# Kernel optimization log

Measured on AMD Instinct MI355X. Metric: run time of the kernel, lower is better.

## Reference

```python
import jax, jax.numpy as jnp
import numpy as np

# Math note: feat = cat([ctx_i, asp_j, ctx_i*asp_j]) dotted with w_u [6H,1]
# decomposes as ctx_i.w1 + asp_j.w2 + (ctx_i*asp_j).w3 where w_u = cat([w1,w2,w3]).
# This lets us compute the full [B, L1, L2] alignment matrix with three small
# contractions instead of L1*L2 concat+matmul launches, with identical math.

def setup_inputs() -> dict:
    key = jax.random.key(0)
    k1, k2, k3 = jax.random.split(key, 3)
    B, L1, L2, D = 64, 512, 32, 600  # D = 2*hidden_dim
    ctx = jax.random.normal(k1, (B, L1, D), dtype=jnp.float32)
    asp = jax.random.normal(k2, (B, L2, D), dtype=jnp.float32)
    w_u = jax.random.normal(k3, (3 * D, 1), dtype=jnp.float32)
    return {"batch_size": B, "ctx": ctx, "asp": asp, "w_u": w_u}

def reference(batch_size, ctx, asp, w_u):
    D = ctx.shape[-1]
    w = w_u[:, 0]
    w1, w2, w3 = w[:D], w[D:2 * D], w[2 * D:]
    ctx_term = ctx @ w1                                  # [B, L1]
    asp_term = asp @ w2                                  # [B, L2]
    cross = jnp.einsum('bid,bjd->bij', ctx * w3, asp)    # [B, L1, L2]
    return ctx_term[:, :, None] + asp_term[:, None, :] + cross
```

## Files before the change

kernel.cpp:

```cpp
#include <hip/hip_runtime.h>
#include <hip/hip_bf16.h>

typedef float  f32x4  __attribute__((ext_vector_type(4)));
typedef short  bf16x8 __attribute__((ext_vector_type(8)));
typedef short  s16x4  __attribute__((ext_vector_type(4)));

#define NB   64
#define NL1  512
#define NL2  32
#define ND   600
#define NDP  640
#define NW1  608
#define ROWS 64

static __device__ __forceinline__ short f2bf(float f) {
    __hip_bfloat16 h = __float2bfloat16(f);
    return __builtin_bit_cast(short, h);
}

__global__ __launch_bounds__(256, 2)
void align_kernel(const float* __restrict__ ctx,
                  const float* __restrict__ asp,
                  const float* __restrict__ wu,
                  float* __restrict__ out)
{
    __shared__ short aspw3[NL2 * NDP];
    __shared__ short w1bf[NW1];
    __shared__ float aspterm[NL2];

    const int tid     = threadIdx.x;
    const int lane    = tid & 63;
    const int wid     = tid >> 6;
    const int b       = blockIdx.x;
    const int rowbase = blockIdx.y * ROWS;

    const int r16 = lane & 15;
    const int g   = lane >> 4;
    const int jx  = lane & 7;
    const float* actx = ctx + ((size_t)b * NL1 + rowbase + wid * 16 + r16) * ND + 8 * g;

    float4 v0 = *(const float4*)(actx);
    float4 v1 = *(const float4*)(actx + 4);
    float4 n0 = *(const float4*)(actx + 32);
    float4 n1 = *(const float4*)(actx + 36);

    for (int i = tid; i < NW1; i += 256)
        w1bf[i] = (i < ND) ? f2bf(wu[i]) : (short)0;

    {
        const int j   = tid >> 3;
        const int e   = tid & 7;
        const int jxs = j & 7;

        aspw3[j * NDP + ((75 ^ jxs) << 3) + e] = 0;

        const int sub = tid & 7;
        const float* arow = asp + ((size_t)b * NL2 + j) * ND;
        float at = 0.f;
        #pragma unroll
        for (int m = 0; m < 19; ++m) {
            const int k = m * 32 + sub * 4;
            if (k < ND) {
                const float4 v  = *(const float4*)(arow + k);
                const float4 w2 = *(const float4*)(wu + ND + k);
                const float4 w3 = *(const float4*)(wu + 2 * ND + k);
                at += v.x * w2.x + v.y * w2.y + v.z * w2.z + v.w * w2.w;
                s16x4 h;
                h.x = f2bf(v.x * w3.x);
                h.y = f2bf(v.y * w3.y);
                h.z = f2bf(v.z * w3.z);
                h.w = f2bf(v.w * w3.w);
                const int c = (k >> 3) ^ jxs;
                *(s16x4*)&aspw3[j * NDP + (c << 3) + (k & 7)] = h;
            }
        }
        at += __shfl_xor(at, 1);
        at += __shfl_xor(at, 2);
        at += __shfl_xor(at, 4);
        if (sub == 0) aspterm[j] = at;
    }
    __syncthreads();

    f32x4 acc0 = {0.f, 0.f, 0.f, 0.f};
    f32x4 acc1 = {0.f, 0.f, 0.f, 0.f};
    f32x4 acc2 = {0.f, 0.f, 0.f, 0.f};

    #pragma unroll 1
    for (int s = 0; s < 19; ++s) {
        float4 p0 = make_float4(0.f, 0.f, 0.f, 0.f);
        float4 p1 = make_float4(0.f, 0.f, 0.f, 0.f);
        if (s < 16) {
            p0 = *(const float4*)(actx + (s + 2) * 32);
            p1 = *(const float4*)(actx + (s + 2) * 32 + 4);
        } else if (s == 16) {
            if (g < 3) {
                p0 = *(const float4*)(actx + 18 * 32);
                p1 = *(const float4*)(actx + 18 * 32 + 4);
            }
        }

        const int k0 = s * 32;
        bf16x8 af;
        af[0] = f2bf(v0.x); af[1] = f2bf(v0.y); af[2] = f2bf(v0.z); af[3] = f2bf(v0.w);
        af[4] = f2bf(v1.x); af[5] = f2bf(v1.y); af[6] = f2bf(v1.z); af[7] = f2bf(v1.w);
        const int c = ((s * 4 + g) ^ jx) << 3;
        const bf16x8 b0 = *(const bf16x8*)&aspw3[r16 * NDP + c];
        const bf16x8 b1 = *(const bf16x8*)&aspw3[(16 + r16) * NDP + c];
        const bf16x8 wf = *(const bf16x8*)&w1bf[k0 + 8 * g];
        acc0 = __builtin_amdgcn_mfma_f32_16x16x32_bf16(af, b0, acc0, 0, 0, 0);
        acc1 = __builtin_amdgcn_mfma_f32_16x16x32_bf16(af, b1, acc1, 0, 0, 0);
        acc2 = __builtin_amdgcn_mfma_f32_16x16x32_bf16(af, wf, acc2, 0, 0, 0);

        v0 = n0; v1 = n1;
        n0 = p0; n1 = p1;
    }

    const float atj0 = aspterm[r16];
    const float atj1 = aspterm[16 + r16];
    float* orow = out + ((size_t)b * NL1 + rowbase + wid * 16 + g * 4) * NL2;
    #pragma unroll
    for (int r = 0; r < 4; ++r) {
        const float cterm = acc2[r];
        orow[r * NL2 + r16]      = acc0[r] + cterm + atj0;
        orow[r * NL2 + 16 + r16] = acc1[r] + cterm + atj1;
    }
}

extern "C" void kernel_launch(void* const* d_in, const int* in_sizes, int n_in,
                              void* d_out, int out_size, void* d_ws, size_t ws_size,
                              hipStream_t stream) {
    (void)in_sizes; (void)n_in; (void)d_ws; (void)ws_size; (void)out_size;
    const float* ctx = (const float*)d_in[1];
    const float* asp = (const float*)d_in[2];
    const float* wu  = (const float*)d_in[3];
    float* out = (float*)d_out;
    dim3 grid(NB, NL1 / ROWS);
    align_kernel<<<grid, 256, 0, stream>>>(ctx, asp, wu, out);
}
```

Measured before the change: 21.84 us.

## Split K across two waves and stream asp from global instead of LDS staging

Replaces the per-block LDS staging of bf16 asp*w3 with direct global loads of asp fragments. The w3 scaling moves onto the ctx operand, and the asp term is computed via an extra MFMA against w2. Blocks shrink to 16 rows and 128 threads, with the two waves splitting the K dimension and reducing through a small LDS buffer. This removes the serial staging prologue and raises occupancy. In exchange, asp is re-read by many more blocks and each wave does more bf16 conversions per step.

```diff
diff --git a/kernel.cpp b/kernel.cpp
--- a/kernel.cpp
+++ b/kernel.cpp
@@ -3,126 +3,127 @@
 
 typedef float  f32x4  __attribute__((ext_vector_type(4)));
 typedef short  bf16x8 __attribute__((ext_vector_type(8)));
-typedef short  s16x4  __attribute__((ext_vector_type(4)));
 
 #define NB   64
 #define NL1  512
 #define NL2  32
 #define ND   600
-#define NDP  640
-#define NW1  608
-#define ROWS 64
+#define NW   608
 
 static __device__ __forceinline__ short f2bf(float f) {
     __hip_bfloat16 h = __float2bfloat16(f);
     return __builtin_bit_cast(short, h);
 }
 
-__global__ __launch_bounds__(256, 2)
+__global__ __launch_bounds__(128, 4)
 void align_kernel(const float* __restrict__ ctx,
                   const float* __restrict__ asp,
                   const float* __restrict__ wu,
                   float* __restrict__ out)
 {
-    __shared__ short aspw3[NL2 * NDP];
-    __shared__ short w1bf[NW1];
-    __shared__ float aspterm[NL2];
+    __shared__ short w1bf[NW];
+    __shared__ short w2bf[NW];
+    __shared__ float w3s[NW];
+    __shared__ float comb[64][15];
 
     const int tid     = threadIdx.x;
     const int lane    = tid & 63;
-    const int wid     = tid >> 6;
+    const int kh      = tid >> 6;
     const int b       = blockIdx.x;
-    const int rowbase = blockIdx.y * ROWS;
+    const int rowbase = blockIdx.y * 16;
 
     const int r16 = lane & 15;
     const int g   = lane >> 4;
-    const int jx  = lane & 7;
-    const float* actx = ctx + ((size_t)b * NL1 + rowbase + wid * 16 + r16) * ND + 8 * g;
 
-    float4 v0 = *(const float4*)(actx);
-    float4 v1 = *(const float4*)(actx + 4);
-    float4 n0 = *(const float4*)(actx + 32);
-    float4 n1 = *(const float4*)(actx + 36);
+    const float* actx = ctx + ((size_t)b * NL1 + rowbase + r16) * ND + 8 * g;
+    const float* aspb = asp + ((size_t)b * NL2 + r16) * ND + 8 * g;
 
-    for (int i = tid; i < NW1; i += 256)
-        w1bf[i] = (i < ND) ? f2bf(wu[i]) : (short)0;
+    const int sbeg = kh ? 10 : 0;
+    const int send = kh ? 19 : 10;
 
-    {
-        const int j   = tid >> 3;
-        const int e   = tid & 7;
-        const int jxs = j & 7;
+#define ISSUE(t, C0, C1, A0, A1, B0, B1)                                   \
+    if ((t) <= 17 || ((t) == 18 && g < 3)) {                               \
+        C0 = *(const float4*)(actx + (t) * 32);                            \
+        C1 = *(const float4*)(actx + (t) * 32 + 4);                        \
+        A0 = *(const float4*)(aspb + (t) * 32);                            \
+        A1 = *(const float4*)(aspb + (t) * 32 + 4);                        \
+        B0 = *(const float4*)(aspb + 16 * ND + (t) * 32);                  \
+        B1 = *(const float4*)(aspb + 16 * ND + (t) * 32 + 4);              \
+    } else {                                                               \
+        C0 = C1 = A0 = A1 = B0 = B1 = make_float4(0.f, 0.f, 0.f, 0.f);    \
+    }
 
-        aspw3[j * NDP + ((75 ^ jxs) << 3) + e] = 0;
+    float4 c0, c1, a0, a1, b0, b1;
+    ISSUE(sbeg, c0, c1, a0, a1, b0, b1)
 
-        const int sub = tid & 7;
-        const float* arow = asp + ((size_t)b * NL2 + j) * ND;
-        float at = 0.f;
-        #pragma unroll
-        for (int m = 0; m < 19; ++m) {
-            const int k = m * 32 + sub * 4;
-            if (k < ND) {
-                const float4 v  = *(const float4*)(arow + k);
-                const float4 w2 = *(const float4*)(wu + ND + k);
-                const float4 w3 = *(const float4*)(wu + 2 * ND + k);
-                at += v.x * w2.x + v.y * w2.y + v.z * w2.z + v.w * w2.w;
-                s16x4 h;
-                h.x = f2bf(v.x * w3.x);
-                h.y = f2bf(v.y * w3.y);
-                h.z = f2bf(v.z * w3.z);
-                h.w = f2bf(v.w * w3.w);
-                const int c = (k >> 3) ^ jxs;
-                *(s16x4*)&aspw3[j * NDP + (c << 3) + (k & 7)] = h;
-            }
-        }
-        at += __shfl_xor(at, 1);
-        at += __shfl_xor(at, 2);
-        at += __shfl_xor(at, 4);
-        if (sub == 0) aspterm[j] = at;
+    for (int i = tid; i < NW; i += 128) {
+        const bool v = i < ND;
+        w1bf[i] = v ? f2bf(wu[i])        : (short)0;
+        w2bf[i] = v ? f2bf(wu[ND + i])   : (short)0;
+        w3s[i]  = v ? wu[2 * ND + i]     : 0.f;
     }
     __syncthreads();
 
-    f32x4 acc0 = {0.f, 0.f, 0.f, 0.f};
-    f32x4 acc1 = {0.f, 0.f, 0.f, 0.f};
-    f32x4 acc2 = {0.f, 0.f, 0.f, 0.f};
+    f32x4 acc0 = {0,0,0,0};
+    f32x4 acc1 = {0,0,0,0};
+    f32x4 acc2 = {0,0,0,0};
+    f32x4 acc3 = {0,0,0,0};
+    f32x4 acc4 = {0,0,0,0};
 
     #pragma unroll 1
-    for (int s = 0; s < 19; ++s) {
-        float4 p0 = make_float4(0.f, 0.f, 0.f, 0.f);
-        float4 p1 = make_float4(0.f, 0.f, 0.f, 0.f);
-        if (s < 16) {
-            p0 = *(const float4*)(actx + (s + 2) * 32);
-            p1 = *(const float4*)(actx + (s + 2) * 32 + 4);
-        } else if (s == 16) {
-            if (g < 3) {
-                p0 = *(const float4*)(actx + 18 * 32);
-                p1 = *(const float4*)(actx + 18 * 32 + 4);
-            }
+    for (int s = sbeg; s < send; ++s) {
+        float4 nc0, nc1, na0, na1, nb0, nb1;
+        ISSUE(s + 1, nc0, nc1, na0, na1, nb0, nb1)
+
+        const int k0g = s * 32 + 8 * g;
+        const bf16x8 wf  = *(const bf16x8*)&w1bf[k0g];
+        const bf16x8 w2f = *(const bf16x8*)&w2bf[k0g];
+        const float4 w3a = *(const float4*)&w3s[k0g];
+        const float4 w3b = *(const float4*)&w3s[k0g + 4];
+
+        bf16x8 af, afw, f0, f1;
+        af[0]  = f2bf(c0.x);        af[1]  = f2bf(c0.y);
+        af[2]  = f2bf(c0.z);        af[3]  = f2bf(c0.w);
+        af[4]  = f2bf(c1.x);        af[5]  = f2bf(c1.y);
+        af[6]  = f2bf(c1.z);        af[7]  = f2bf(c1.w);
+        afw[0] = f2bf(c0.x * w3a.x); afw[1] = f2bf(c0.y * w3a.y);
+        afw[2] = f2bf(c0.z * w3a.z); afw[3] = f2bf(c0.w * w3a.w);
+        afw[4] = f2bf(c1.x * w3b.x); afw[5] = f2bf(c1.y * w3b.y);
+        afw[6] = f2bf(c1.z * w3b.z); afw[7] = f2bf(c1.w * w3b.w);
+        f0[0] = f2bf(a0.x); f0[1] = f2bf(a0.y); f0[2] = f2bf(a0.z); f0[3] = f2bf(a0.w);
+        f0[4] = f2bf(a1.x); f0[5] = f2bf(a1.y); f0[6] = f2bf(a1.z); f0[7] = f2bf(a1.w);
+        f1[0] = f2bf(b0.x); f1[1] = f2bf(b0.y); f1[2] = f2bf(b0.z); f1[3] = f2bf(b0.w);
+        f1[4] = f2bf(b1.x); f1[5] = f2bf(b1.y); f1[6] = f2bf(b1.z); f1[7] = f2bf(b1.w);
+
+        acc0 = __builtin_amdgcn_mfma_f32_16x16x32_bf16(afw, f0, acc0, 0, 0, 0);
+        acc1 = __builtin_amdgcn_mfma_f32_16x16x32_bf16(afw, f1, acc1, 0, 0, 0);
+        acc2 = __builtin_amdgcn_mfma_f32_16x16x32_bf16(af,  wf, acc2, 0, 0, 0);
+        acc3 = __builtin_amdgcn_mfma_f32_16x16x32_bf16(w2f, f0, acc3, 0, 0, 0);
+        acc4 = __builtin_amdgcn_mfma_f32_16x16x32_bf16(w2f, f1, acc4, 0, 0, 0);
+
+        c0 = nc0; c1 = nc1; a0 = na0; a1 = na1; b0 = nb0; b1 = nb1;
+    }
+#undef ISSUE
+
+    if (kh == 1) {
+        float* c = comb[lane];
+        c[0]  = acc0[0]; c[1]  = acc0[1]; c[2]  = acc0[2]; c[3]  = acc0[3];
+        c[4]  = acc1[0]; c[5]  = acc1[1]; c[6]  = acc1[2]; c[7]  = acc1[3];
+        c[8]  = acc2[0]; c[9]  = acc2[1]; c[10] = acc2[2]; c[11] = acc2[3];
+        c[12] = acc3[0]; c[13] = acc4[0];
+    }
+    __syncthreads();
+    if (kh == 0) {
+        const float* c = comb[lane];
+        const float atj0 = acc3[0] + c[12];
+        const float atj1 = acc4[0] + c[13];
+        float* orow = out + ((size_t)b * NL1 + rowbase + g * 4) * NL2;
+        #pragma unroll
+        for (int r = 0; r < 4; ++r) {
+            const float ct = acc2[r] + c[8 + r];
+            orow[r * NL2 + r16]      = acc0[r] + c[r]     + ct + atj0;
+            orow[r * NL2 + 16 + r16] = acc1[r] + c[4 + r] + ct + atj1;
         }
-
-        const int k0 = s * 32;
-        bf16x8 af;
-        af[0] = f2bf(v0.x); af[1] = f2bf(v0.y); af[2] = f2bf(v0.z); af[3] = f2bf(v0.w);
-        af[4] = f2bf(v1.x); af[5] = f2bf(v1.y); af[6] = f2bf(v1.z); af[7] = f2bf(v1.w);
-        const int c = ((s * 4 + g) ^ jx) << 3;
-        const bf16x8 b0 = *(const bf16x8*)&aspw3[r16 * NDP + c];
-        const bf16x8 b1 = *(const bf16x8*)&aspw3[(16 + r16) * NDP + c];
-        const bf16x8 wf = *(const bf16x8*)&w1bf[k0 + 8 * g];
-        acc0 = __builtin_amdgcn_mfma_f32_16x16x32_bf16(af, b0, acc0, 0, 0, 0);
-        acc1 = __builtin_amdgcn_mfma_f32_16x16x32_bf16(af, b1, acc1, 0, 0, 0);
-        acc2 = __builtin_amdgcn_mfma_f32_16x16x32_bf16(af, wf, acc2, 0, 0, 0);
-
-        v0 = n0; v1 = n1;
-        n0 = p0; n1 = p1;
-    }
-
-    const float atj0 = aspterm[r16];
-    const float atj1 = aspterm[16 + r16];
-    float* orow = out + ((size_t)b * NL1 + rowbase + wid * 16 + g * 4) * NL2;
-    #pragma unroll
-    for (int r = 0; r < 4; ++r) {
-        const float cterm = acc2[r];
-        orow[r * NL2 + r16]      = acc0[r] + cterm + atj0;
-        orow[r * NL2 + 16 + r16] = acc1[r] + cterm + atj1;
     }
 }
 
@@ -134,6 +135,6 @@
     const float* asp = (const float*)d_in[2];
     const float* wu  = (const float*)d_in[3];
     float* out = (float*)d_out;
-    dim3 grid(NB, NL1 / ROWS);
-    align_kernel<<<grid, 256, 0, stream>>>(ctx, asp, wu, out);
+    dim3 grid(NB, NL1 / 16);
+    align_kernel<<<grid, 128, 0, stream>>>(ctx, asp, wu, out);
 }
```

Result: slower. 28.01 us (+28.2%).

## Split asp/w3 prep into separate kernel writing MFMA-ready bf16 panels

Applied to the files above, without the earlier changes.

Adds a prep kernel that builds per-batch bf16 asp*w3 panels, the bf16 w1 vector and partial asp·w2 sums in workspace, laid out in MFMA fragment order. The main kernel then loads B fragments straight from global memory instead of having every block redo the prep in LDS behind a __syncthreads. The main loop is unrolled by two with double-buffered register prefetch. This removes prep work repeated 8x per batch and the LDS barrier, but adds a second launch and a workspace round trip.

```diff
diff --git a/kernel.cpp b/kernel.cpp
--- a/kernel.cpp
+++ b/kernel.cpp
@@ -9,115 +9,158 @@
 #define NL1  512
 #define NL2  32
 #define ND   600
-#define NDP  640
-#define NW1  608
-#define ROWS 64
+#define PBATCH 19456
+#define PANEL_SH ((size_t)NB * PBATCH)
+#define W1P_OFF  PANEL_SH
+#define AT4_OFF  (PANEL_SH + 608)
 
 static __device__ __forceinline__ short f2bf(float f) {
     __hip_bfloat16 h = __float2bfloat16(f);
     return __builtin_bit_cast(short, h);
 }
 
+__global__ __launch_bounds__(256, 4)
+void prep_kernel(const float* __restrict__ asp,
+                 const float* __restrict__ wu,
+                 short* __restrict__ ws_sh)
+{
+    short* panel = ws_sh;
+    short* w1p   = ws_sh + W1P_OFF;
+    float* at4   = (float*)(ws_sh + AT4_OFF);
+
+    const int b    = blockIdx.x;
+    const int q    = blockIdx.y;
+    const int sbeg = q * 5;
+    const int send = (q == 3) ? 19 : sbeg + 5;
+    const int tid  = threadIdx.x;
+    const int j    = tid >> 3;
+    const int sub  = tid & 7;
+    const int gq   = sub >> 1;
+    const int e4   = (sub & 1) * 4;
+    const int half = j >> 4;
+    const int r    = j & 15;
+
+    const float* arow = asp + ((size_t)b * NL2 + j) * ND;
+    short* pb = panel + (size_t)b * PBATCH;
+
+    float at = 0.f;
+    #pragma unroll
+    for (int s = sbeg; s < send; ++s) {
+        const int k = s * 32 + sub * 4;
+        if (k < ND) {
+            const float4 v  = *(const float4*)(arow + k);
+            const float4 w2 = *(const float4*)(wu + ND + k);
+            const float4 w3 = *(const float4*)(wu + 2 * ND + k);
+            at += v.x * w2.x + v.y * w2.y + v.z * w2.z + v.w * w2.w;
+            s16x4 h;
+            h.x = f2bf(v.x * w3.x);
+            h.y = f2bf(v.y * w3.y);
+            h.z = f2bf(v.z * w3.z);
+            h.w = f2bf(v.w * w3.w);
+            *(s16x4*)&pb[(((s * 2 + half) * 4 + gq) * 16 + r) * 8 + e4] = h;
+        }
+    }
+    at += __shfl_xor(at, 1);
+    at += __shfl_xor(at, 2);
+    at += __shfl_xor(at, 4);
+    if (sub == 0) at4[((size_t)b * 4 + q) * NL2 + j] = at;
+
+    if (q == 3) {
+        if (tid < 32) {
+            const int hh = tid >> 4, rr = tid & 15;
+            #pragma unroll
+            for (int e = 0; e < 8; ++e)
+                pb[(((18 * 2 + hh) * 4 + 3) * 16 + rr) * 8 + e] = 0;
+        }
+        if (b == 0 && tid < 76) {
+            const int s = tid >> 2, gg = tid & 3;
+            #pragma unroll
+            for (int e = 0; e < 8; ++e) {
+                const int k = s * 32 + gg * 8 + e;
+                w1p[(s * 4 + gg) * 8 + e] = (k < ND) ? f2bf(wu[k]) : (short)0;
+            }
+        }
+    }
+}
+
 __global__ __launch_bounds__(256, 2)
 void align_kernel(const float* __restrict__ ctx,
-                  const float* __restrict__ asp,
-                  const float* __restrict__ wu,
+                  const short* __restrict__ ws_sh,
                   float* __restrict__ out)
 {
-    __shared__ short aspw3[NL2 * NDP];
-    __shared__ short w1bf[NW1];
-    __shared__ float aspterm[NL2];
+    const short* panel = ws_sh;
+    const short* w1p   = ws_sh + W1P_OFF;
+    const float* at4   = (const float*)(ws_sh + AT4_OFF);
 
     const int tid     = threadIdx.x;
     const int lane    = tid & 63;
     const int wid     = tid >> 6;
     const int b       = blockIdx.x;
-    const int rowbase = blockIdx.y * ROWS;
+    const int rowbase = blockIdx.y * 64 + wid * 16;
 
     const int r16 = lane & 15;
     const int g   = lane >> 4;
-    const int jx  = lane & 7;
-    const float* actx = ctx + ((size_t)b * NL1 + rowbase + wid * 16 + r16) * ND + 8 * g;
 
-    float4 v0 = *(const float4*)(actx);
-    float4 v1 = *(const float4*)(actx + 4);
-    float4 n0 = *(const float4*)(actx + 32);
-    float4 n1 = *(const float4*)(actx + 36);
+    const float* actx = ctx + ((size_t)b * NL1 + rowbase + r16) * ND + 8 * g;
+    const short* pb   = panel + (size_t)b * PBATCH;
 
-    for (int i = tid; i < NW1; i += 256)
-        w1bf[i] = (i < ND) ? f2bf(wu[i]) : (short)0;
+#define ISSUE_C(t, C0, C1)                                                     \
+    if ((t) <= 17 || ((t) == 18 && g < 3)) {                                   \
+        C0 = *(const float4*)(actx + (t) * 32);                                \
+        C1 = *(const float4*)(actx + (t) * 32 + 4);                            \
+    } else if ((t) == 18) {                                                    \
+        C0 = make_float4(0.f, 0.f, 0.f, 0.f);                                  \
+        C1 = make_float4(0.f, 0.f, 0.f, 0.f);                                  \
+    }
 
-    {
-        const int j   = tid >> 3;
-        const int e   = tid & 7;
-        const int jxs = j & 7;
+#define ISSUE_B(t, F0, F1, WF)                                                 \
+    if ((t) <= 18) {                                                           \
+        F0 = *(const bf16x8*)&pb[(t) * 1024 + lane * 8];                       \
+        F1 = *(const bf16x8*)&pb[(t) * 1024 + 512 + lane * 8];                 \
+        WF = *(const bf16x8*)&w1p[((t) * 4 + g) * 8];                          \
+    }
 
-        aspw3[j * NDP + ((75 ^ jxs) << 3) + e] = 0;
+    float4 cA0, cA1, cB0, cB1;
+    bf16x8 fA0, fA1, wA, fB0, fB1, wB;
+    ISSUE_C(0, cA0, cA1) ISSUE_B(0, fA0, fA1, wA)
+    ISSUE_C(1, cB0, cB1) ISSUE_B(1, fB0, fB1, wB)
 
-        const int sub = tid & 7;
-        const float* arow = asp + ((size_t)b * NL2 + j) * ND;
-        float at = 0.f;
-        #pragma unroll
-        for (int m = 0; m < 19; ++m) {
-            const int k = m * 32 + sub * 4;
-            if (k < ND) {
-                const float4 v  = *(const float4*)(arow + k);
-                const float4 w2 = *(const float4*)(wu + ND + k);
-                const float4 w3 = *(const float4*)(wu + 2 * ND + k);
-                at += v.x * w2.x + v.y * w2.y + v.z * w2.z + v.w * w2.w;
-                s16x4 h;
-                h.x = f2bf(v.x * w3.x);
-                h.y = f2bf(v.y * w3.y);
-                h.z = f2bf(v.z * w3.z);
-                h.w = f2bf(v.w * w3.w);
-                const int c = (k >> 3) ^ jxs;
-                *(s16x4*)&aspw3[j * NDP + (c << 3) + (k & 7)] = h;
-            }
-        }
-        at += __shfl_xor(at, 1);
-        at += __shfl_xor(at, 2);
-        at += __shfl_xor(at, 4);
-        if (sub == 0) aspterm[j] = at;
+    f32x4 acc0 = {0,0,0,0};
+    f32x4 acc1 = {0,0,0,0};
+    f32x4 acc2 = {0,0,0,0};
+
+#define STEP(s, C0, C1, F0, F1, WF)                                            \
+    {                                                                          \
+        bf16x8 af;                                                             \
+        af[0] = f2bf(C0.x); af[1] = f2bf(C0.y);                                \
+        af[2] = f2bf(C0.z); af[3] = f2bf(C0.w);                                \
+        af[4] = f2bf(C1.x); af[5] = f2bf(C1.y);                                \
+        af[6] = f2bf(C1.z); af[7] = f2bf(C1.w);                                \
+        acc0 = __builtin_amdgcn_mfma_f32_16x16x32_bf16(af, F0, acc0, 0, 0, 0); \
+        acc1 = __builtin_amdgcn_mfma_f32_16x16x32_bf16(af, F1, acc1, 0, 0, 0); \
+        acc2 = __builtin_amdgcn_mfma_f32_16x16x32_bf16(af, WF, acc2, 0, 0, 0); \
+        ISSUE_C((s) + 2, C0, C1)                                               \
+        ISSUE_B((s) + 2, F0, F1, WF)                                           \
     }
-    __syncthreads();
-
-    f32x4 acc0 = {0.f, 0.f, 0.f, 0.f};
-    f32x4 acc1 = {0.f, 0.f, 0.f, 0.f};
-    f32x4 acc2 = {0.f, 0.f, 0.f, 0.f};
 
     #pragma unroll 1
-    for (int s = 0; s < 19; ++s) {
-        float4 p0 = make_float4(0.f, 0.f, 0.f, 0.f);
-        float4 p1 = make_float4(0.f, 0.f, 0.f, 0.f);
-        if (s < 16) {
-            p0 = *(const float4*)(actx + (s + 2) * 32);
-            p1 = *(const float4*)(actx + (s + 2) * 32 + 4);
-        } else if (s == 16) {
-            if (g < 3) {
-                p0 = *(const float4*)(actx + 18 * 32);
-                p1 = *(const float4*)(actx + 18 * 32 + 4);
-            }
-        }
+    for (int s = 0; s < 18; s += 2) {
+        STEP(s,     cA0, cA1, fA0, fA1, wA)
+        STEP(s + 1, cB0, cB1, fB0, fB1, wB)
+    }
+    STEP(18, cA0, cA1, fA0, fA1, wA)
 
-        const int k0 = s * 32;
-        bf16x8 af;
-        af[0] = f2bf(v0.x); af[1] = f2bf(v0.y); af[2] = f2bf(v0.z); af[3] = f2bf(v0.w);
-        af[4] = f2bf(v1.x); af[5] = f2bf(v1.y); af[6] = f2bf(v1.z); af[7] = f2bf(v1.w);
-        const int c = ((s * 4 + g) ^ jx) << 3;
-        const bf16x8 b0 = *(const bf16x8*)&aspw3[r16 * NDP + c];
-        const bf16x8 b1 = *(const bf16x8*)&aspw3[(16 + r16) * NDP + c];
-        const bf16x8 wf = *(const bf16x8*)&w1bf[k0 + 8 * g];
-        acc0 = __builtin_amdgcn_mfma_f32_16x16x32_bf16(af, b0, acc0, 0, 0, 0);
-        acc1 = __builtin_amdgcn_mfma_f32_16x16x32_bf16(af, b1, acc1, 0, 0, 0);
-        acc2 = __builtin_amdgcn_mfma_f32_16x16x32_bf16(af, wf, acc2, 0, 0, 0);
+#undef STEP
+#undef ISSUE_B
+#undef ISSUE_C
 
-        v0 = n0; v1 = n1;
-        n0 = p0; n1 = p1;
+    float atj0 = 0.f, atj1 = 0.f;
+    #pragma unroll
+    for (int q = 0; q < 4; ++q) {
+        atj0 += at4[((size_t)b * 4 + q) * NL2 + r16];
+        atj1 += at4[((size_t)b * 4 + q) * NL2 + 16 + r16];
     }
-
-    const float atj0 = aspterm[r16];
-    const float atj1 = aspterm[16 + r16];
-    float* orow = out + ((size_t)b * NL1 + rowbase + wid * 16 + g * 4) * NL2;
+    float* orow = out + ((size_t)b * NL1 + rowbase + g * 4) * NL2;
     #pragma unroll
     for (int r = 0; r < 4; ++r) {
         const float cterm = acc2[r];
@@ -129,11 +172,15 @@
 extern "C" void kernel_launch(void* const* d_in, const int* in_sizes, int n_in,
                               void* d_out, int out_size, void* d_ws, size_t ws_size,
                               hipStream_t stream) {
-    (void)in_sizes; (void)n_in; (void)d_ws; (void)ws_size; (void)out_size;
+    (void)in_sizes; (void)n_in; (void)ws_size; (void)out_size;
     const float* ctx = (const float*)d_in[1];
     const float* asp = (const float*)d_in[2];
     const float* wu  = (const float*)d_in[3];
     float* out = (float*)d_out;
-    dim3 grid(NB, NL1 / ROWS);
-    align_kernel<<<grid, 256, 0, stream>>>(ctx, asp, wu, out);
+    short* ws_sh = (short*)d_ws;
+
+    dim3 g1(NB, 4);
+    prep_kernel<<<g1, 256, 0, stream>>>(asp, wu, ws_sh);
+    dim3 g2(NB, NL1 / 64);
+    align_kernel<<<g2, 256, 0, stream>>>(ctx, ws_sh, out);
 }
```

New measurement: 23.47 us. 7.4% more time.

## Split K dimension across two wave groups with LDS reduction

Applied to the files above, without the earlier changes.

Doubles the block to 512 threads and splits the 600-wide reduction into two halves, each handled by a separate group of four waves. Partial accumulators are combined through a shared-memory buffer before the epilogue writes the output. The asp preprocessing is spread over 16 threads per row, and ctx loads become nontemporal with a one-step prefetch instead of two. This aims to raise memory-level parallelism and shorten the serial per-wave K loop, at the cost of an extra barrier, LDS traffic and higher per-block resource use.

```diff
diff --git a/kernel.cpp b/kernel.cpp
--- a/kernel.cpp
+++ b/kernel.cpp
@@ -11,14 +11,13 @@
 #define ND   600
 #define NDP  640
 #define NW1  608
-#define ROWS 64
 
 static __device__ __forceinline__ short f2bf(float f) {
     __hip_bfloat16 h = __float2bfloat16(f);
     return __builtin_bit_cast(short, h);
 }
 
-__global__ __launch_bounds__(256, 2)
+__global__ __launch_bounds__(512, 2)
 void align_kernel(const float* __restrict__ ctx,
                   const float* __restrict__ asp,
                   const float* __restrict__ wu,
@@ -27,39 +26,56 @@
     __shared__ short aspw3[NL2 * NDP];
     __shared__ short w1bf[NW1];
     __shared__ float aspterm[NL2];
+    __shared__ float comb[4][64][12];
 
-    const int tid     = threadIdx.x;
-    const int lane    = tid & 63;
-    const int wid     = tid >> 6;
-    const int b       = blockIdx.x;
-    const int rowbase = blockIdx.y * ROWS;
+    const int tid   = threadIdx.x;
+    const int lane  = tid & 63;
+    const int w     = tid >> 6;
+    const int strip = w & 3;
+    const int kh    = w >> 2;
+    const int b     = blockIdx.x;
+    const int rowbase = blockIdx.y * 64 + strip * 16;
 
     const int r16 = lane & 15;
     const int g   = lane >> 4;
     const int jx  = lane & 7;
-    const float* actx = ctx + ((size_t)b * NL1 + rowbase + wid * 16 + r16) * ND + 8 * g;
 
-    float4 v0 = *(const float4*)(actx);
-    float4 v1 = *(const float4*)(actx + 4);
-    float4 n0 = *(const float4*)(actx + 32);
-    float4 n1 = *(const float4*)(actx + 36);
+    const float* actx = ctx + ((size_t)b * NL1 + rowbase + r16) * ND + 8 * g;
+    const int sbeg = kh ? 10 : 0;
+    const int send = kh ? 19 : 10;
 
-    for (int i = tid; i < NW1; i += 256)
+#define ISSUE_C(t, C0, C1) do {                                                \
+        const int _t = (t);                                                    \
+        if (_t < send) {                                                       \
+            if (_t <= 17 || g < 3) {                                           \
+                C0 = __builtin_nontemporal_load((const f32x4*)(actx + _t * 32));      \
+                C1 = __builtin_nontemporal_load((const f32x4*)(actx + _t * 32 + 4));  \
+            } else {                                                           \
+                C0 = (f32x4){0.f,0.f,0.f,0.f};                                 \
+                C1 = (f32x4){0.f,0.f,0.f,0.f};                                 \
+            }                                                                  \
+        }                                                                      \
+    } while (0)
+
+    f32x4 v0 = {0.f,0.f,0.f,0.f}, v1 = {0.f,0.f,0.f,0.f};
+    ISSUE_C(sbeg, v0, v1);
+
+    for (int i = tid; i < NW1; i += 512)
         w1bf[i] = (i < ND) ? f2bf(wu[i]) : (short)0;
 
     {
-        const int j   = tid >> 3;
-        const int e   = tid & 7;
+        const int j   = tid >> 4;
+        const int sub = tid & 15;
         const int jxs = j & 7;
 
-        aspw3[j * NDP + ((75 ^ jxs) << 3) + e] = 0;
+        if (sub < 8)
+            aspw3[j * NDP + ((75 ^ jxs) << 3) + sub] = 0;
 
-        const int sub = tid & 7;
         const float* arow = asp + ((size_t)b * NL2 + j) * ND;
         float at = 0.f;
         #pragma unroll
-        for (int m = 0; m < 19; ++m) {
-            const int k = m * 32 + sub * 4;
+        for (int m = 0; m < 10; ++m) {
+            const int k = m * 64 + sub * 4;
             if (k < ND) {
                 const float4 v  = *(const float4*)(arow + k);
                 const float4 w2 = *(const float4*)(wu + ND + k);
@@ -77,52 +93,54 @@
         at += __shfl_xor(at, 1);
         at += __shfl_xor(at, 2);
         at += __shfl_xor(at, 4);
+        at += __shfl_xor(at, 8);
         if (sub == 0) aspterm[j] = at;
     }
     __syncthreads();
 
-    f32x4 acc0 = {0.f, 0.f, 0.f, 0.f};
-    f32x4 acc1 = {0.f, 0.f, 0.f, 0.f};
-    f32x4 acc2 = {0.f, 0.f, 0.f, 0.f};
+    f32x4 acc0 = {0,0,0,0};
+    f32x4 acc1 = {0,0,0,0};
+    f32x4 acc2 = {0,0,0,0};
 
     #pragma unroll 1
-    for (int s = 0; s < 19; ++s) {
-        float4 p0 = make_float4(0.f, 0.f, 0.f, 0.f);
-        float4 p1 = make_float4(0.f, 0.f, 0.f, 0.f);
-        if (s < 16) {
-            p0 = *(const float4*)(actx + (s + 2) * 32);
-            p1 = *(const float4*)(actx + (s + 2) * 32 + 4);
-        } else if (s == 16) {
-            if (g < 3) {
-                p0 = *(const float4*)(actx + 18 * 32);
-                p1 = *(const float4*)(actx + 18 * 32 + 4);
-            }
-        }
+    for (int s = sbeg; s < send; ++s) {
+        f32x4 n0 = {0.f,0.f,0.f,0.f}, n1 = {0.f,0.f,0.f,0.f};
+        ISSUE_C(s + 1, n0, n1);
 
-        const int k0 = s * 32;
         bf16x8 af;
         af[0] = f2bf(v0.x); af[1] = f2bf(v0.y); af[2] = f2bf(v0.z); af[3] = f2bf(v0.w);
         af[4] = f2bf(v1.x); af[5] = f2bf(v1.y); af[6] = f2bf(v1.z); af[7] = f2bf(v1.w);
-        const int c = ((s * 4 + g) ^ jx) << 3;
-        const bf16x8 b0 = *(const bf16x8*)&aspw3[r16 * NDP + c];
-        const bf16x8 b1 = *(const bf16x8*)&aspw3[(16 + r16) * NDP + c];
-        const bf16x8 wf = *(const bf16x8*)&w1bf[k0 + 8 * g];
-        acc0 = __builtin_amdgcn_mfma_f32_16x16x32_bf16(af, b0, acc0, 0, 0, 0);
-        acc1 = __builtin_amdgcn_mfma_f32_16x16x32_bf16(af, b1, acc1, 0, 0, 0);
+        const int cB = ((s * 4 + g) ^ jx) << 3;
+        const bf16x8 f0 = *(const bf16x8*)&aspw3[r16 * NDP + cB];
+        const bf16x8 f1 = *(const bf16x8*)&aspw3[(16 + r16) * NDP + cB];
+        const bf16x8 wf = *(const bf16x8*)&w1bf[s * 32 + 8 * g];
+        acc0 = __builtin_amdgcn_mfma_f32_16x16x32_bf16(af, f0, acc0, 0, 0, 0);
+        acc1 = __builtin_amdgcn_mfma_f32_16x16x32_bf16(af, f1, acc1, 0, 0, 0);
         acc2 = __builtin_amdgcn_mfma_f32_16x16x32_bf16(af, wf, acc2, 0, 0, 0);
 
         v0 = n0; v1 = n1;
-        n0 = p0; n1 = p1;
     }
+#undef ISSUE_C
 
-    const float atj0 = aspterm[r16];
-    const float atj1 = aspterm[16 + r16];
-    float* orow = out + ((size_t)b * NL1 + rowbase + wid * 16 + g * 4) * NL2;
-    #pragma unroll
-    for (int r = 0; r < 4; ++r) {
-        const float cterm = acc2[r];
-        orow[r * NL2 + r16]      = acc0[r] + cterm + atj0;
-        orow[r * NL2 + 16 + r16] = acc1[r] + cterm + atj1;
+    if (kh == 1) {
+        *(f32x4*)&comb[strip][lane][0] = acc0;
+        *(f32x4*)&comb[strip][lane][4] = acc1;
+        *(f32x4*)&comb[strip][lane][8] = acc2;
+    }
+    __syncthreads();
+    if (kh == 0) {
+        const f32x4 c0s = *(const f32x4*)&comb[strip][lane][0];
+        const f32x4 c1s = *(const f32x4*)&comb[strip][lane][4];
+        const f32x4 c2s = *(const f32x4*)&comb[strip][lane][8];
+        const float atj0 = aspterm[r16];
+        const float atj1 = aspterm[16 + r16];
+        float* orow = out + ((size_t)b * NL1 + rowbase + g * 4) * NL2;
+        #pragma unroll
+        for (int r = 0; r < 4; ++r) {
+            const float ct = acc2[r] + c2s[r];
+            orow[r * NL2 + r16]      = acc0[r] + c0s[r] + ct + atj0;
+            orow[r * NL2 + 16 + r16] = acc1[r] + c1s[r] + ct + atj1;
+        }
     }
 }
 
@@ -134,6 +152,6 @@
     const float* asp = (const float*)d_in[2];
     const float* wu  = (const float*)d_in[3];
     float* out = (float*)d_out;
-    dim3 grid(NB, NL1 / ROWS);
-    align_kernel<<<grid, 256, 0, stream>>>(ctx, asp, wu, out);
+    dim3 grid(NB, NL1 / 64);
+    align_kernel<<<grid, 512, 0, stream>>>(ctx, asp, wu, out);
 }
```

After: 32.06 us. +46.8%, slower.
